# Performance work log

Measured on AMD Instinct MI355X. Metric: run time of the kernel, lower is better.

The kernel has to match this reference:

```python
import jax, jax.numpy as jnp
import numpy as np

N = 50000      # nodes
E = 800000     # random edges (self-loops appended, per PyG add_self_loops=True)
IN = 256       # input_dim
HID = 64       # hidden_dim (per-head out_channels)
H = 4          # heads (hardcoded in GAT)
OUT = 64       # output_dim
NEG_SLOPE = 0.2  # PyG GATv2Conv default negative_slope


def setup_inputs() -> dict:
    key = jax.random.key(0)
    ks = jax.random.split(key, 24)
    g = lambda i, shape: jax.random.normal(ks[i], shape, jnp.float32) * 0.05
    inp = {
        "x": jax.random.normal(ks[0], (N, IN), jnp.float32),
        "edge_index": jax.random.randint(ks[1], (2, E), 0, N, dtype=jnp.int32),
        # conv1: GATv2Conv(IN, HID, heads=4)
        "W1l": g(2, (IN, H * HID)), "b1l": g(3, (H * HID,)),
        "W1r": g(4, (IN, H * HID)), "b1r": g(5, (H * HID,)),
        "att1": g(6, (H, HID)), "bias1": g(7, (H * HID,)),
        # conv2: GATv2Conv(4*HID, HID, heads=4)
        "W2l": g(8, (H * HID, H * HID)), "b2l": g(9, (H * HID,)),
        "W2r": g(10, (H * HID, H * HID)), "b2r": g(11, (H * HID,)),
        "att2": g(12, (H, HID)), "bias2": g(13, (H * HID,)),
        # post_mp: Linear(4*HID, HID) -> Dropout -> Linear(HID, OUT)
        "Wp1": g(14, (H * HID, HID)), "bp1": g(15, (HID,)),
        "Wp2": g(16, (HID, OUT)), "bp2": g(17, (OUT,)),
    }
    return inp


def _gatv2_layer(x, src, dst, Wl, bl, Wr, br, att, bias):
    # GATv2Conv (concat=True): x_l = lin_l(x) for sources, x_r = lin_r(x) for targets
    C = att.shape[1]
    xl = (x @ Wl + bl).reshape(-1, H, C)   # [N,H,C]
    xr = (x @ Wr + br).reshape(-1, H, C)
    e = jax.nn.leaky_relu(xl[src] + xr[dst], NEG_SLOPE)     # [E',H,C]
    logits = jnp.einsum('ehc,hc->eh', e, att)               # [E',H]
    # segment softmax over destination nodes (self-loops guarantee nonempty segments)
    m = jax.ops.segment_max(logits, dst, num_segments=N)
    p = jnp.exp(logits - m[dst])
    s = jax.ops.segment_sum(p, dst, num_segments=N)
    alpha = p / s[dst]                                      # [E',H]
    out = jax.ops.segment_sum(xl[src] * alpha[..., None], dst, num_segments=N)
    return out.reshape(-1, H * C) + bias                    # [N,H*C]


def reference(x, edge_index, W1l, b1l, W1r, b1r, att1, bias1,
              W2l, b2l, W2r, b2r, att2, bias2, Wp1, bp1, Wp2, bp2):
    # add self-loops (PyG GATv2Conv default add_self_loops=True)
    loops = jnp.arange(N, dtype=edge_index.dtype)
    src = jnp.concatenate([edge_index[0], loops])
    dst = jnp.concatenate([edge_index[1], loops])
    h = _gatv2_layer(x, src, dst, W1l, b1l, W1r, b1r, att1, bias1)
    h = jax.nn.relu(h)  # dropout p=0.6 is identity in eval mode
    h = _gatv2_layer(h, src, dst, W2l, b2l, W2r, b2r, att2, bias2)
    h = jax.nn.relu(h)
    h = h @ Wp1 + bp1   # post_mp (dropout identity in eval)
    h = h @ Wp2 + bp2
    return h
```

## Files before the change

kernel.cpp:

```cpp
#include <hip/hip_runtime.h>

typedef unsigned short u16;
typedef short bf16x8 __attribute__((ext_vector_type(8)));
typedef float f32x4 __attribute__((ext_vector_type(4)));

__device__ __forceinline__ u16 f2bf(float f) {
    unsigned u = __float_as_uint(f);
    return (u16)((u + 0x7fffu + ((u >> 16) & 1u)) >> 16);
}
__device__ __forceinline__ float exp2_hw(float x) {
    float r;
    asm("v_exp_f32 %0, %1" : "=v"(r) : "v"(x));
    return r;
}
template <int CTRL>
__device__ __forceinline__ float dpp_add(float p) {
    int t = __builtin_amdgcn_update_dpp(0, __float_as_int(p), CTRL, 0xf, 0xf, true);
    return p + __int_as_float(t);
}
__device__ __forceinline__ void gload_lds16(const u16* g, u16* lds) {
    __builtin_amdgcn_global_load_lds((const __attribute__((address_space(1))) void*)g,
                                     (__attribute__((address_space(3))) void*)lds, 16, 0, 0);
}

struct MegaP {
    const float* x; const int* ei;
    const float *W1l, *b1l, *W1r, *b1r, *att1, *bias1;
    const float *W2l, *b2l, *W2r, *b2r, *att2, *bias2;
    const float *Wp1, *bp1, *Wp2, *bp2;
    u16 *Abuf, *XLR, *WB1, *WB2, *Wpt;
    float *bc1, *bc2, *bpf;
    int *cnt, *slot;
    float* outF;
    int N, E, Mpad, Mt;
};


template <bool AF32, int BN, bool F32OUT>
__device__ __forceinline__ void gemm_tile(const void* __restrict__ Av, const u16* __restrict__ Bt,
                                          const float* __restrict__ bias, void* __restrict__ out,
                                          int M, int Nout, int bm, int bn, u16* As, u16* Bs) {
    constexpr int K = 256;
    constexpr int NRF = BN / 64;
    const int tid = threadIdx.x;
    const int l = tid & 63;
    const int w = tid >> 6;
    const int wm = w >> 2, wn = w & 3;
    const int lrow = l & 15, lk = l >> 4;
    const int wbase = tid & ~63;

#pragma unroll
    for (int it = 0; it < BN / 16; ++it) {
        int c = it * 512 + tid;
        int col = c >> 5, kc = c & 31;
        bf16x8 v = *(const bf16x8*)(Bt + (size_t)(bn * BN + col) * K + kc * 8);
        *(bf16x8*)(Bs + col * K + ((kc ^ (col & 7)) * 8)) = v;
    }

    auto stageA = [&](int ks) {
        if (AF32) {
            const float* A32 = (const float*)Av;
#pragma unroll
            for (int it = 0; it < 2; ++it) {
                int c = it * 512 + tid;
                int row = c >> 3, seg = c & 7;
                int grow = bm * 128 + row;
                if (grow > M - 1) grow = M - 1;
                const float* sp = A32 + (size_t)grow * K + ks * 64 + seg * 8;
                float4 v0 = *(const float4*)sp;
                float4 v1 = *(const float4*)(sp + 4);
                bf16x8 pk;
                pk[0] = (short)f2bf(v0.x); pk[1] = (short)f2bf(v0.y);
                pk[2] = (short)f2bf(v0.z); pk[3] = (short)f2bf(v0.w);
                pk[4] = (short)f2bf(v1.x); pk[5] = (short)f2bf(v1.y);
                pk[6] = (short)f2bf(v1.z); pk[7] = (short)f2bf(v1.w);
                *(bf16x8*)(As + row * 64 + ((seg ^ (row & 7)) * 8)) = pk;
            }
        } else {
            const u16* Abf = (const u16*)Av;
#pragma unroll
            for (int it = 0; it < 2; ++it) {
                int c = it * 512 + tid;
                int row = c >> 3, seg = c & 7;
                int ssrc = seg ^ (row & 7);
                gload_lds16(Abf + (size_t)(bm * 128 + row) * K + ks * 64 + ssrc * 8,
                            As + (size_t)(it * 512 + wbase) * 8);
            }
        }
    };

    f32x4 acc[4][NRF];
#pragma unroll
    for (int m = 0; m < 4; ++m)
#pragma unroll
        for (int n = 0; n < NRF; ++n) acc[m][n] = (f32x4){0.f, 0.f, 0.f, 0.f};

    stageA(0);
    __syncthreads();

    for (int ks = 0; ks < 4; ++ks) {
#pragma unroll
        for (int h = 0; h < 2; ++h) {
            bf16x8 av[4], bv[NRF];
#pragma unroll
            for (int m = 0; m < 4; ++m) {
                int row = wm * 64 + m * 16 + lrow;
                int seg = ((h * 4 + lk) ^ (row & 7));
                av[m] = *(const bf16x8*)(As + row * 64 + seg * 8);
            }
#pragma unroll
            for (int n = 0; n < NRF; ++n) {
                int col = wn * (NRF * 16) + n * 16 + lrow;
                int kc = ks * 8 + h * 4 + lk;
                bv[n] = *(const bf16x8*)(Bs + col * K + ((kc ^ (col & 7)) * 8));
            }
#pragma unroll
            for (int m = 0; m < 4; ++m)
#pragma unroll
                for (int n = 0; n < NRF; ++n)
                    acc[m][n] = __builtin_amdgcn_mfma_f32_16x16x32_bf16(av[m], bv[n], acc[m][n], 0, 0, 0);
        }
        if (ks < 3) {
            __syncthreads();
            stageA(ks + 1);
            __syncthreads();
        }
    }

    float bl[NRF];
#pragma unroll
    for (int n = 0; n < NRF; ++n) bl[n] = bias[bn * BN + wn * (NRF * 16) + n * 16 + lrow];

#pragma unroll
    for (int m = 0; m < 4; ++m) {
        int grow = bm * 128 + wm * 64 + m * 16 + lk * 4;
#pragma unroll
        for (int j = 0; j < 4; ++j) {
            if (grow + j < M) {
#pragma unroll
                for (int n = 0; n < NRF; ++n) {
                    int col = bn * BN + wn * (NRF * 16) + n * 16 + lrow;
                    float v = acc[m][n][j] + bl[n];
                    if (F32OUT)
                        ((float*)out)[(size_t)(grow + j) * Nout + col] = v;
                    else
                        ((u16*)out)[(size_t)(grow + j) * Nout + col] = f2bf(v);
                }
            }
        }
    }
}

__device__ __forceinline__ void tile_map4(int d, int Mt, int& bm, int& bn) {
    int nfull = (Mt & ~7) * 4;
    if (d < nfull) {
        int g = d >> 5, r = d & 31;
        bm = g * 8 + (r & 7);
        bn = r >> 3;
    } else {
        int idx = d - nfull;
        bm = (Mt & ~7) + (idx >> 2);
        bn = idx & 3;
    }
}


__global__ __launch_bounds__(256) void k_prep(MegaP P) {
    const int N = P.N, E = P.E, EP = E + N;
    const int nAdj = (EP + 255) / 256;
    const int c0 = 1024, c1 = c0 + 64, c2 = c1 + nAdj;
    int b = blockIdx.x;
    int tid = threadIdx.x;
    if (b < c0) {
        int n = b & 255, m = b >> 8;
        const float* W = (m == 0) ? P.W1l : (m == 1) ? P.W1r : (m == 2) ? P.W2l : P.W2r;
        u16* dst = (m < 2) ? P.WB1 : P.WB2;
        dst[(size_t)((m & 1) * 256 + n) * 256 + tid] = f2bf(W[(size_t)tid * 256 + n]);
    } else if (b < c1) {
        int j = b - c0;
        float a = 0.f;
        for (int k = 0; k < 64; ++k) a += P.Wp1[tid * 64 + k] * P.Wp2[k * 64 + j];
        P.Wpt[j * 256 + tid] = f2bf(a);
        if (tid == 0) {
            float bb = P.bp2[j];
            for (int k = 0; k < 64; ++k) bb += P.bp1[k] * P.Wp2[k * 64 + j];
            P.bpf[j] = bb;
        }
    } else if (b < c2) {
        int e = (b - c1) * 256 + tid;
        if (e < EP) {
            int src, dst;
            if (e < E) { src = P.ei[e]; dst = P.ei[E + e]; }
            else       { src = e - E; dst = e - E; }
            int p = atomicAdd(P.cnt + dst, 1);
            if (p < 64) P.slot[((size_t)dst << 6) + p] = src;
        }
    } else {
        int m = b - c2;
        const float* s = (m == 0) ? P.b1l : (m == 1) ? P.b1r : (m == 2) ? P.b2l : P.b2r;
        float* d = (m < 2) ? P.bc1 : P.bc2;
        d[(m & 1) * 256 + tid] = s[tid];
    }
}


__global__ __launch_bounds__(512) void k_g1(MegaP P) {
    __shared__ __align__(16) u16 As[8192];
    __shared__ __align__(16) u16 Bs[32768];
    int bm, bn;
    tile_map4(blockIdx.x, P.Mt, bm, bn);
    gemm_tile<true, 128, false>(P.x, P.WB1, P.bc1, P.XLR, P.N, 512, bm, bn, As, Bs);
}

__global__ __launch_bounds__(512) void k_g2(MegaP P) {
    __shared__ __align__(16) u16 As[8192];
    __shared__ __align__(16) u16 Bs[32768];
    int bm, bn;
    tile_map4(blockIdx.x, P.Mt, bm, bn);
    gemm_tile<false, 128, false>(P.Abuf, P.WB2, P.bc2, P.XLR, P.N, 512, bm, bn, As, Bs);
}

__global__ __launch_bounds__(512) void k_gp(MegaP P) {
    __shared__ __align__(16) u16 As[8192];
    __shared__ __align__(16) u16 Bs[16384];
    gemm_tile<false, 64, true>(P.Abuf, P.Wpt, P.bpf, P.outF, P.N, 64, blockIdx.x, 0, As, Bs);
}


__global__ __launch_bounds__(256) void k_edge(const int* __restrict__ cnt,
                                              const int* __restrict__ slot,
                                              const u16* __restrict__ XLR,
                                              const float* __restrict__ att,
                                              const float* __restrict__ bias,
                                              u16* __restrict__ H, int N) {
    int wid0 = blockIdx.x * 4 + (threadIdx.x >> 6);
    if (wid0 >= N) return;
    const int wid = __builtin_amdgcn_readfirstlane(wid0);
    const int l = threadIdx.x & 63;

    const float LOG2E = 1.4426950408889634f;
    float4 a4 = *(const float4*)(att + l * 4);
    a4.x *= LOG2E; a4.y *= LOG2E; a4.z *= LOG2E; a4.w *= LOG2E;
    float4 bb = *(const float4*)(bias + l * 4);
    const char* Xb = (const char*)XLR;
    const int lofs = l << 3;

    uint2 xr = *(const uint2*)(Xb + ((size_t)wid << 10) + 512 + lofs);
    float r0 = __uint_as_float(xr.x << 16), r1 = __uint_as_float(xr.x & 0xffff0000u);
    float r2 = __uint_as_float(xr.y << 16), r3 = __uint_as_float(xr.y & 0xffff0000u);

    const int* sl = slot + ((size_t)wid << 6);
    int deg = cnt[wid];
    if (deg > 64) deg = 64;
    float s = 0.f, o0 = 0.f, o1 = 0.f, o2 = 0.f, o3 = 0.f;

    auto edge1 = [&](uint2 wv) {
        float c0 = __uint_as_float(wv.x << 16), c1 = __uint_as_float(wv.x & 0xffff0000u);
        float c2 = __uint_as_float(wv.y << 16), c3 = __uint_as_float(wv.y & 0xffff0000u);
        float t0 = c0 + r0, t1 = c1 + r1, t2 = c2 + r2, t3 = c3 + r3;
        t0 = fmaf(-0.8f, fminf(t0, 0.f), t0);
        t1 = fmaf(-0.8f, fminf(t1, 0.f), t1);
        t2 = fmaf(-0.8f, fminf(t2, 0.f), t2);
        t3 = fmaf(-0.8f, fminf(t3, 0.f), t3);
        float p = t0 * a4.x; p = fmaf(t1, a4.y, p); p = fmaf(t2, a4.z, p); p = fmaf(t3, a4.w, p);
        p = dpp_add<0xB1>(p);
        p = dpp_add<0x4E>(p);
        p = dpp_add<0x141>(p);
        p = dpp_add<0x140>(p);
        float e = exp2_hw(p);
        s += e;
        o0 = fmaf(e, c0, o0); o1 = fmaf(e, c1, o1);
        o2 = fmaf(e, c2, o2); o3 = fmaf(e, c3, o3);
    };

    int i = 0;
    for (; i + 8 <= deg; i += 8) {
        int u0 = __builtin_amdgcn_readfirstlane(sl[i]);
        int u1 = __builtin_amdgcn_readfirstlane(sl[i + 1]);
        int u2 = __builtin_amdgcn_readfirstlane(sl[i + 2]);
        int u3 = __builtin_amdgcn_readfirstlane(sl[i + 3]);
        int u4 = __builtin_amdgcn_readfirstlane(sl[i + 4]);
        int u5 = __builtin_amdgcn_readfirstlane(sl[i + 5]);
        int u6 = __builtin_amdgcn_readfirstlane(sl[i + 6]);
        int u7 = __builtin_amdgcn_readfirstlane(sl[i + 7]);
        uint2 w0 = *(const uint2*)(Xb + ((size_t)u0 << 10) + lofs);
        uint2 w1 = *(const uint2*)(Xb + ((size_t)u1 << 10) + lofs);
        uint2 w2 = *(const uint2*)(Xb + ((size_t)u2 << 10) + lofs);
        uint2 w3 = *(const uint2*)(Xb + ((size_t)u3 << 10) + lofs);
        uint2 w4 = *(const uint2*)(Xb + ((size_t)u4 << 10) + lofs);
        uint2 w5 = *(const uint2*)(Xb + ((size_t)u5 << 10) + lofs);
        uint2 w6 = *(const uint2*)(Xb + ((size_t)u6 << 10) + lofs);
        uint2 w7 = *(const uint2*)(Xb + ((size_t)u7 << 10) + lofs);
        edge1(w0); edge1(w1); edge1(w2); edge1(w3);
        edge1(w4); edge1(w5); edge1(w6); edge1(w7);
    }
    for (; i + 4 <= deg; i += 4) {
        int u0 = __builtin_amdgcn_readfirstlane(sl[i]);
        int u1 = __builtin_amdgcn_readfirstlane(sl[i + 1]);
        int u2 = __builtin_amdgcn_readfirstlane(sl[i + 2]);
        int u3 = __builtin_amdgcn_readfirstlane(sl[i + 3]);
        uint2 w0 = *(const uint2*)(Xb + ((size_t)u0 << 10) + lofs);
        uint2 w1 = *(const uint2*)(Xb + ((size_t)u1 << 10) + lofs);
        uint2 w2 = *(const uint2*)(Xb + ((size_t)u2 << 10) + lofs);
        uint2 w3 = *(const uint2*)(Xb + ((size_t)u3 << 10) + lofs);
        edge1(w0); edge1(w1); edge1(w2); edge1(w3);
    }
    for (; i < deg; ++i) {
        int u0 = __builtin_amdgcn_readfirstlane(sl[i]);
        uint2 w0 = *(const uint2*)(Xb + ((size_t)u0 << 10) + lofs);
        edge1(w0);
    }

    float inv = 1.f / s;
    o0 = fmaxf(fmaf(o0, inv, bb.x), 0.f);
    o1 = fmaxf(fmaf(o1, inv, bb.y), 0.f);
    o2 = fmaxf(fmaf(o2, inv, bb.z), 0.f);
    o3 = fmaxf(fmaf(o3, inv, bb.w), 0.f);
    ushort4 w4 = {f2bf(o0), f2bf(o1), f2bf(o2), f2bf(o3)};
    *(ushort4*)(H + ((size_t)wid << 8) + l * 4) = w4;
}


extern "C" void kernel_launch(void* const* d_in, const int* in_sizes, int n_in,
                              void* d_out, int out_size, void* d_ws, size_t ws_size,
                              hipStream_t stream) {
    MegaP P;
    P.x     = (const float*)d_in[0];
    P.ei    = (const int*)d_in[1];
    P.W1l   = (const float*)d_in[2];  P.b1l  = (const float*)d_in[3];
    P.W1r   = (const float*)d_in[4];  P.b1r  = (const float*)d_in[5];
    P.att1  = (const float*)d_in[6];  P.bias1 = (const float*)d_in[7];
    P.W2l   = (const float*)d_in[8];  P.b2l  = (const float*)d_in[9];
    P.W2r   = (const float*)d_in[10]; P.b2r  = (const float*)d_in[11];
    P.att2  = (const float*)d_in[12]; P.bias2 = (const float*)d_in[13];
    P.Wp1   = (const float*)d_in[14]; P.bp1  = (const float*)d_in[15];
    P.Wp2   = (const float*)d_in[16]; P.bp2  = (const float*)d_in[17];

    const int N = in_sizes[0] / 256;
    const int E = in_sizes[1] / 2;
    const int EP = E + N;
    const int Mpad = ((N + 127) / 128) * 128;

    char* ws = (char*)d_ws;
    size_t o = 0;
    auto alloc = [&](size_t b) { char* p = ws + o; o = (o + b + 255) & ~(size_t)255; return p; };
    P.Abuf   = (u16*)alloc((size_t)Mpad * 256 * 2);
    P.XLR    = (u16*)alloc((size_t)Mpad * 512 * 2);
    P.WB1    = (u16*)alloc(512 * 256 * 2);
    P.WB2    = (u16*)alloc(512 * 256 * 2);
    P.Wpt    = (u16*)alloc(64 * 256 * 2);
    P.bc1    = (float*)alloc(512 * 4);
    P.bc2    = (float*)alloc(512 * 4);
    P.bpf    = (float*)alloc(64 * 4);
    P.cnt    = (int*)alloc((size_t)N * 4);
    P.slot   = (int*)alloc((size_t)N * 64 * 4);
    P.outF   = (float*)d_out;
    P.N = N; P.E = E; P.Mpad = Mpad; P.Mt = Mpad / 128;

    hipMemsetAsync(P.cnt, 0, (size_t)N * 4, stream);
    if (Mpad > N)
        hipMemsetAsync(P.Abuf + (size_t)N * 256, 0, (size_t)(Mpad - N) * 256 * 2, stream);

    const int nAdj = (EP + 255) / 256;
    k_prep<<<1024 + 64 + nAdj + 4, 256, 0, stream>>>(P);

    const int ntile = P.Mt * 4;
    const int egrid = (N + 3) / 4;
    k_g1<<<ntile, 512, 0, stream>>>(P);
    k_edge<<<egrid, 256, 0, stream>>>(P.cnt, P.slot, P.XLR, P.att1, P.bias1, P.Abuf, N);
    k_g2<<<ntile, 512, 0, stream>>>(P);
    k_edge<<<egrid, 256, 0, stream>>>(P.cnt, P.slot, P.XLR, P.att2, P.bias2, P.Abuf, N);
    k_gp<<<P.Mt, 512, 0, stream>>>(P);
}
```

Measured before the change: 265.6 us.

## Overlap adjacency build with first GEMM and shrink slot indices to 16-bit

Moves the edge bucketing (atomic count and slot fill) out of the prep kernel into the first GEMM launch, so adjacency blocks run alongside the layer-1 projection tiles. The two memsets are folded into the prep kernel as zeroing blocks, which removes separate API calls. Slot indices are stored as u16, halving slot traffic, but this only holds if node ids fit in 16 bits; N=50000 does, larger graphs would break. The combined kernel mixes atomic scatter blocks with 512-thread GEMM blocks that carry large LDS, which may affect occupancy for the adjacency part.

```diff
diff --git a/kernel.cpp b/kernel.cpp
--- a/kernel.cpp
+++ b/kernel.cpp
@@ -30,7 +30,7 @@
     const float *Wp1, *bp1, *Wp2, *bp2;
     u16 *Abuf, *XLR, *WB1, *WB2, *Wpt;
     float *bc1, *bc2, *bpf;
-    int *cnt, *slot;
+    int *cnt; u16 *slot;
     float* outF;
     int N, E, Mpad, Mt;
 };
@@ -166,9 +166,9 @@
 
 
 __global__ __launch_bounds__(256) void k_prep(MegaP P) {
-    const int N = P.N, E = P.E, EP = E + N;
-    const int nAdj = (EP + 255) / 256;
-    const int c0 = 1024, c1 = c0 + 64, c2 = c1 + nAdj;
+    const int N = P.N;
+    const int nZc = (N + 255) / 256;
+    const int c0 = 1024, c1 = c0 + 64, c2 = c1 + 4, c3 = c2 + nZc;
     int b = blockIdx.x;
     int tid = threadIdx.x;
     if (b < c0) {
@@ -187,29 +187,38 @@
             P.bpf[j] = bb;
         }
     } else if (b < c2) {
-        int e = (b - c1) * 256 + tid;
+        int m = b - c1;
+        const float* s = (m == 0) ? P.b1l : (m == 1) ? P.b1r : (m == 2) ? P.b2l : P.b2r;
+        float* d = (m < 2) ? P.bc1 : P.bc2;
+        d[(m & 1) * 256 + tid] = s[tid];
+    } else if (b < c3) {
+        int i = (b - c2) * 256 + tid;
+        if (i < N) P.cnt[i] = 0;
+    } else {
+        int i = (b - c3) * 256 + tid;
+        P.Abuf[(size_t)N * 256 + i] = 0;
+    }
+}
+
+
+__global__ __launch_bounds__(512) void k_ga1(MegaP P, int nAdj) {
+    __shared__ __align__(16) u16 As[8192];
+    __shared__ __align__(16) u16 Bs[32768];
+    if ((int)blockIdx.x < nAdj) {
+        const int E = P.E, EP = E + P.N;
+        int e = (int)blockIdx.x * 512 + threadIdx.x;
         if (e < EP) {
             int src, dst;
             if (e < E) { src = P.ei[e]; dst = P.ei[E + e]; }
             else       { src = e - E; dst = e - E; }
             int p = atomicAdd(P.cnt + dst, 1);
-            if (p < 64) P.slot[((size_t)dst << 6) + p] = src;
+            if (p < 64) P.slot[((size_t)dst << 6) + p] = (u16)src;
         }
     } else {
-        int m = b - c2;
-        const float* s = (m == 0) ? P.b1l : (m == 1) ? P.b1r : (m == 2) ? P.b2l : P.b2r;
-        float* d = (m < 2) ? P.bc1 : P.bc2;
-        d[(m & 1) * 256 + tid] = s[tid];
-    }
-}
-
-
-__global__ __launch_bounds__(512) void k_g1(MegaP P) {
-    __shared__ __align__(16) u16 As[8192];
-    __shared__ __align__(16) u16 Bs[32768];
-    int bm, bn;
-    tile_map4(blockIdx.x, P.Mt, bm, bn);
-    gemm_tile<true, 128, false>(P.x, P.WB1, P.bc1, P.XLR, P.N, 512, bm, bn, As, Bs);
+        int bm, bn;
+        tile_map4((int)blockIdx.x - nAdj, P.Mt, bm, bn);
+        gemm_tile<true, 128, false>(P.x, P.WB1, P.bc1, P.XLR, P.N, 512, bm, bn, As, Bs);
+    }
 }
 
 __global__ __launch_bounds__(512) void k_g2(MegaP P) {
@@ -228,7 +237,7 @@
 
 
 __global__ __launch_bounds__(256) void k_edge(const int* __restrict__ cnt,
-                                              const int* __restrict__ slot,
+                                              const u16* __restrict__ slot,
                                               const u16* __restrict__ XLR,
                                               const float* __restrict__ att,
                                               const float* __restrict__ bias,
@@ -249,7 +258,7 @@
     float r0 = __uint_as_float(xr.x << 16), r1 = __uint_as_float(xr.x & 0xffff0000u);
     float r2 = __uint_as_float(xr.y << 16), r3 = __uint_as_float(xr.y & 0xffff0000u);
 
-    const int* sl = slot + ((size_t)wid << 6);
+    const u16* sl = slot + ((size_t)wid << 6);
     int deg = cnt[wid];
     if (deg > 64) deg = 64;
     float s = 0.f, o0 = 0.f, o1 = 0.f, o2 = 0.f, o3 = 0.f;
@@ -353,20 +362,19 @@
     P.bc2    = (float*)alloc(512 * 4);
     P.bpf    = (float*)alloc(64 * 4);
     P.cnt    = (int*)alloc((size_t)N * 4);
-    P.slot   = (int*)alloc((size_t)N * 64 * 4);
+    P.slot   = (u16*)alloc((size_t)N * 64 * 2);
     P.outF   = (float*)d_out;
     P.N = N; P.E = E; P.Mpad = Mpad; P.Mt = Mpad / 128;
 
-    hipMemsetAsync(P.cnt, 0, (size_t)N * 4, stream);
-    if (Mpad > N)
-        hipMemsetAsync(P.Abuf + (size_t)N * 256, 0, (size_t)(Mpad - N) * 256 * 2, stream);
-
-    const int nAdj = (EP + 255) / 256;
-    k_prep<<<1024 + 64 + nAdj + 4, 256, 0, stream>>>(P);
-
+    const int nZc = (N + 255) / 256;
+    const int nZp = Mpad - N;
+    k_prep<<<1024 + 64 + 4 + nZc + nZp, 256, 0, stream>>>(P);
+
+    const int nAdj = (EP + 511) / 512;
     const int ntile = P.Mt * 4;
+    k_ga1<<<nAdj + ntile, 512, 0, stream>>>(P, nAdj);
+
     const int egrid = (N + 3) / 4;
-    k_g1<<<ntile, 512, 0, stream>>>(P);
     k_edge<<<egrid, 256, 0, stream>>>(P.cnt, P.slot, P.XLR, P.att1, P.bias1, P.Abuf, N);
     k_g2<<<ntile, 512, 0, stream>>>(P);
     k_edge<<<egrid, 256, 0, stream>>>(P.cnt, P.slot, P.XLR, P.att2, P.bias2, P.Abuf, N);
```

Measured after the change: 275.4 us. 3.7% more time.

## Compact adjacency to u16, partition scatter by XCD, inline self-loops

Applied to the files above, without the earlier changes.

The adjacency slot table now stores 16-bit source indices instead of 32-bit. This halves its footprint and the index traffic in the edge kernels, but only works while N stays below 65536. The scatter is replicated into 8 passes over the edge list, each handling only the destinations in one eighth of the node range. The intent is to keep each node's atomics and slot writes local to one XCD's L2, at the cost of reading the destination array 8 times. Self-loops are no longer inserted into the slot table; each edge kernel processes the node's own feature row up front.

```diff
diff --git a/kernel.cpp b/kernel.cpp
--- a/kernel.cpp
+++ b/kernel.cpp
@@ -30,7 +30,7 @@
     const float *Wp1, *bp1, *Wp2, *bp2;
     u16 *Abuf, *XLR, *WB1, *WB2, *Wpt;
     float *bc1, *bc2, *bpf;
-    int *cnt, *slot;
+    int *cnt; u16 *slot;
     float* outF;
     int N, E, Mpad, Mt;
 };
@@ -166,9 +166,8 @@
 
 
 __global__ __launch_bounds__(256) void k_prep(MegaP P) {
-    const int N = P.N, E = P.E, EP = E + N;
-    const int nAdj = (EP + 255) / 256;
-    const int c0 = 1024, c1 = c0 + 64, c2 = c1 + nAdj;
+    const int N = P.N, E = P.E;
+    const int c0 = 1024, c1 = c0 + 64, c2 = c1 + 4;
     int b = blockIdx.x;
     int tid = threadIdx.x;
     if (b < c0) {
@@ -187,19 +186,23 @@
             P.bpf[j] = bb;
         }
     } else if (b < c2) {
-        int e = (b - c1) * 256 + tid;
-        if (e < EP) {
-            int src, dst;
-            if (e < E) { src = P.ei[e]; dst = P.ei[E + e]; }
-            else       { src = e - E; dst = e - E; }
-            int p = atomicAdd(P.cnt + dst, 1);
-            if (p < 64) P.slot[((size_t)dst << 6) + p] = src;
-        }
-    } else {
-        int m = b - c2;
+        int m = b - c1;
         const float* s = (m == 0) ? P.b1l : (m == 1) ? P.b1r : (m == 2) ? P.b2l : P.b2r;
         float* d = (m < 2) ? P.bc1 : P.bc2;
         d[(m & 1) * 256 + tid] = s[tid];
+    } else {
+        int bi = b - c2;
+        int xcd = bi & 7;
+        int e = (bi >> 3) * 256 + tid;
+        if (e < E) {
+            int dst = P.ei[E + e];
+            int S = (N + 7) >> 3;
+            if ((unsigned)(dst - xcd * S) < (unsigned)S) {
+                int src = P.ei[e];
+                int p = atomicAdd(P.cnt + dst, 1);
+                if (p < 64) P.slot[((size_t)dst << 6) + p] = (u16)src;
+            }
+        }
     }
 }
 
@@ -228,7 +231,7 @@
 
 
 __global__ __launch_bounds__(256) void k_edge(const int* __restrict__ cnt,
-                                              const int* __restrict__ slot,
+                                              const u16* __restrict__ slot,
                                               const u16* __restrict__ XLR,
                                               const float* __restrict__ att,
                                               const float* __restrict__ bias,
@@ -249,7 +252,7 @@
     float r0 = __uint_as_float(xr.x << 16), r1 = __uint_as_float(xr.x & 0xffff0000u);
     float r2 = __uint_as_float(xr.y << 16), r3 = __uint_as_float(xr.y & 0xffff0000u);
 
-    const int* sl = slot + ((size_t)wid << 6);
+    const u16* sl = slot + ((size_t)wid << 6);
     int deg = cnt[wid];
     if (deg > 64) deg = 64;
     float s = 0.f, o0 = 0.f, o1 = 0.f, o2 = 0.f, o3 = 0.f;
@@ -272,6 +275,11 @@
         o0 = fmaf(e, c0, o0); o1 = fmaf(e, c1, o1);
         o2 = fmaf(e, c2, o2); o3 = fmaf(e, c3, o3);
     };
+
+    {
+        uint2 w0 = *(const uint2*)(Xb + ((size_t)wid << 10) + lofs);
+        edge1(w0);
+    }
 
     int i = 0;
     for (; i + 8 <= deg; i += 8) {
@@ -338,7 +346,6 @@
 
     const int N = in_sizes[0] / 256;
     const int E = in_sizes[1] / 2;
-    const int EP = E + N;
     const int Mpad = ((N + 127) / 128) * 128;
 
     char* ws = (char*)d_ws;
@@ -353,7 +360,7 @@
     P.bc2    = (float*)alloc(512 * 4);
     P.bpf    = (float*)alloc(64 * 4);
     P.cnt    = (int*)alloc((size_t)N * 4);
-    P.slot   = (int*)alloc((size_t)N * 64 * 4);
+    P.slot   = (u16*)alloc((size_t)N * 64 * 2);
     P.outF   = (float*)d_out;
     P.N = N; P.E = E; P.Mpad = Mpad; P.Mt = Mpad / 128;
 
@@ -361,8 +368,8 @@
     if (Mpad > N)
         hipMemsetAsync(P.Abuf + (size_t)N * 256, 0, (size_t)(Mpad - N) * 256 * 2, stream);
 
-    const int nAdj = (EP + 255) / 256;
-    k_prep<<<1024 + 64 + nAdj + 4, 256, 0, stream>>>(P);
+    const int nScat = ((E + 255) / 256) * 8;
+    k_prep<<<1024 + 64 + 4 + nScat, 256, 0, stream>>>(P);
 
     const int ntile = P.Mt * 4;
     const int egrid = (N + 3) / 4;
```

Result: faster. 249.9 us (median of 2 runs) (-5.9%).
